# Optimization experiments

Hardware: AMD Instinct MI355X
Metric: run time of the kernel (lower is better)

Reference implementation:

```python
import jax, jax.numpy as jnp
import numpy as np

NUM_ROUTING = 3


def squash(v, axis=-1):
    s2 = jnp.sum(jnp.square(v), axis=axis, keepdims=True)
    scale = s2 / (1.0 + s2) / jnp.sqrt(s2 + 1e-7)
    return scale * v


def setup_inputs() -> dict:
    key = jax.random.key(0)
    k1, k2 = jax.random.split(key)
    B, I, D_in, J, D_out = 64, 2304, 8, 32, 16
    inputs = jax.random.normal(k1, (B, I, D_in), dtype=jnp.float32)
    # keras random_uniform(-1, 1)
    W = jax.random.uniform(k2, (I, J, D_in, D_out), dtype=jnp.float32, minval=-1.0, maxval=1.0)
    b0 = jnp.zeros((I, J), dtype=jnp.float32)
    return {"inputs": inputs, "W": W, "b0": b0}


def reference(inputs, W, b0):
    B = inputs.shape[0]
    I, J = b0.shape
    # u_hat[b,i,j,e] = inputs[b,i,:] @ W[i,j,:,e]  -> [B, I, J, E]
    u_hat = jnp.einsum('bid,ijde->bije', inputs, W)
    b = jnp.broadcast_to(b0[None], (B, I, J))
    V = None
    for it in range(NUM_ROUTING):
        c = jax.nn.softmax(b, axis=-1)                      # [B, I, J]
        S = jnp.einsum('bij,bije->bje', c, u_hat)           # [B, J, E]
        V = squash(S)
        if it != NUM_ROUTING - 1:
            b = b + jnp.einsum('bje,bije->bij', V, u_hat)   # agreement update
    return V
```

## Files before the change

### kernel.cpp

```cpp
#include <hip/hip_runtime.h>
#include <hip/hip_fp16.h>

#define I_DIM 2304
#define J_DIM 32
#define D_IN  8
#define E_DIM 16
#define B_DIM 64
#define BJE   (B_DIM * J_DIM * E_DIM)
#define HBJE  (BJE / 2)
#define NC7   256
#define CH7   (I_DIM / NC7)
#define TILEW 4096

typedef const __attribute__((address_space(1))) char* gcp_t;
typedef __attribute__((address_space(3)))       char* lcp_t;

#define DPP_ADD(s, ctrl) ((s) + __int_as_float(__builtin_amdgcn_update_dpp( \
    0, __float_as_int(s), (ctrl), 0xF, 0xF, true)))

template <bool FIRST>
__global__ __launch_bounds__(256, 2) void caps_pass_v22(
    const float* __restrict__ x,
    const float* __restrict__ W,
    const float* __restrict__ b0,
    const float* __restrict__ Vacc,
    __half2* __restrict__ partial)
{
    const int tid   = threadIdx.x;
    const int wv    = __builtin_amdgcn_readfirstlane(tid >> 6);
    const int wvx   = tid >> 6;
    const int lane  = tid & 63;
    const int jj    = lane & 31;
    const int eh    = lane >> 5;
    const int km    = jj & 15;
    const int chunk = blockIdx.x & (NC7 - 1);
    const int qb    = blockIdx.x >> 8;
    const int i0    = chunk * CH7;
    const int bloc0 = wv * 4;
    const int bbase = qb * 16 + bloc0;
    const int bxb   = qb * 16 + wvx * 4;

    __shared__ float Ws[2][TILEW];

    auto stage = [&](int buf, int itile) {
        const char* wt = (const char*)(W + (size_t)itile * TILEW);
#pragma unroll
        for (int r = 0; r < 4; ++r) {
            const int g    = (wv * 4 + r) * 64 + lane;
            const int srcu = (g & ~31) | ((g & 31) ^ ((g >> 5) & 15));
            __builtin_amdgcn_global_load_lds(
                (gcp_t)(wt + (size_t)srcu * 16),
                (lcp_t)((char*)&Ws[buf][(wv * 4 + r) * 256]),
                16, 0, 0);
        }
    };

    stage(0, i0);

    float vacc[4][8];
    if constexpr (!FIRST) {
#pragma unroll
        for (int bb = 0; bb < 4; ++bb) {
            const float* vp = Vacc + ((size_t)((bbase + bb) * J_DIM + jj)) * E_DIM + eh * 8;
            const float4 v0 = *(const float4*)vp;
            const float4 v1 = *(const float4*)(vp + 4);
            vacc[bb][0]=v0.x; vacc[bb][1]=v0.y; vacc[bb][2]=v0.z; vacc[bb][3]=v0.w;
            vacc[bb][4]=v1.x; vacc[bb][5]=v1.y; vacc[bb][6]=v1.z; vacc[bb][7]=v1.w;
        }
    }

    float Sacc[4][8];
#pragma unroll
    for (int bb = 0; bb < 4; ++bb)
#pragma unroll
        for (int e = 0; e < 8; ++e) Sacc[bb][e] = 0.f;

    __syncthreads();

    int cur = 0;
    for (int ii = 0; ii < CH7; ++ii) {
        const int i = i0 + ii;
        if (ii + 1 < CH7) stage(cur ^ 1, i + 1);

        const float b0v = b0[i * J_DIM + jj];

        const float* wb = &Ws[cur][0];

        float uh[4][8];
#pragma unroll
        for (int bb = 0; bb < 4; ++bb)
#pragma unroll
            for (int e = 0; e < 8; ++e) uh[bb][e] = 0.f;

        {
            float xq[4][4];
#pragma unroll
            for (int bb = 0; bb < 4; ++bb) {
                const float4 t = *(const float4*)(x + ((size_t)(bxb + bb) * I_DIM + i) * D_IN);
                xq[bb][0]=t.x; xq[bb][1]=t.y; xq[bb][2]=t.z; xq[bb][3]=t.w;
            }
            float4 w[8];
#pragma unroll
            for (int d = 0; d < 4; ++d) {
                const int u0 = (d << 2) | (eh << 1);
                w[2*d]   = *(const float4*)&wb[jj * 128 + (((u0    ) ^ km) << 2)];
                w[2*d+1] = *(const float4*)&wb[jj * 128 + (((u0 | 1) ^ km) << 2)];
            }
#pragma unroll
            for (int d = 0; d < 4; ++d) {
                const float4 wlo = w[2*d], whi = w[2*d+1];
#pragma unroll
                for (int bb = 0; bb < 4; ++bb) {
                    const float xv = xq[bb][d];
                    uh[bb][0] = fmaf(xv, wlo.x, uh[bb][0]);
                    uh[bb][1] = fmaf(xv, wlo.y, uh[bb][1]);
                    uh[bb][2] = fmaf(xv, wlo.z, uh[bb][2]);
                    uh[bb][3] = fmaf(xv, wlo.w, uh[bb][3]);
                    uh[bb][4] = fmaf(xv, whi.x, uh[bb][4]);
                    uh[bb][5] = fmaf(xv, whi.y, uh[bb][5]);
                    uh[bb][6] = fmaf(xv, whi.z, uh[bb][6]);
                    uh[bb][7] = fmaf(xv, whi.w, uh[bb][7]);
                }
            }
        }
        {
            float xq[4][4];
#pragma unroll
            for (int bb = 0; bb < 4; ++bb) {
                const float4 t = *(const float4*)(x + ((size_t)(bxb + bb) * I_DIM + i) * D_IN + 4);
                xq[bb][0]=t.x; xq[bb][1]=t.y; xq[bb][2]=t.z; xq[bb][3]=t.w;
            }
            float4 w[8];
#pragma unroll
            for (int d = 4; d < 8; ++d) {
                const int u0 = (d << 2) | (eh << 1);
                w[2*(d-4)]   = *(const float4*)&wb[jj * 128 + (((u0    ) ^ km) << 2)];
                w[2*(d-4)+1] = *(const float4*)&wb[jj * 128 + (((u0 | 1) ^ km) << 2)];
            }
#pragma unroll
            for (int d = 0; d < 4; ++d) {
                const float4 wlo = w[2*d], whi = w[2*d+1];
#pragma unroll
                for (int bb = 0; bb < 4; ++bb) {
                    const float xv = xq[bb][d];
                    uh[bb][0] = fmaf(xv, wlo.x, uh[bb][0]);
                    uh[bb][1] = fmaf(xv, wlo.y, uh[bb][1]);
                    uh[bb][2] = fmaf(xv, wlo.z, uh[bb][2]);
                    uh[bb][3] = fmaf(xv, wlo.w, uh[bb][3]);
                    uh[bb][4] = fmaf(xv, whi.x, uh[bb][4]);
                    uh[bb][5] = fmaf(xv, whi.y, uh[bb][5]);
                    uh[bb][6] = fmaf(xv, whi.z, uh[bb][6]);
                    uh[bb][7] = fmaf(xv, whi.w, uh[bb][7]);
                }
            }
        }

#pragma unroll
        for (int bb = 0; bb < 4; ++bb) {
            float l;
            if constexpr (FIRST) {
                l = b0v;
            } else {
                float l0 = 0.f, l1 = 0.f;
#pragma unroll
                for (int e = 0; e < 8; e += 2) {
                    l0 = fmaf(vacc[bb][e],     uh[bb][e],     l0);
                    l1 = fmaf(vacc[bb][e + 1], uh[bb][e + 1], l1);
                }
                float lg = l0 + l1;
                lg += __shfl_xor(lg, 32);
                l = b0v + lg;
            }

            const float p = __expf(l);
            float s = p;
            s = DPP_ADD(s, 0xB1);
            s = DPP_ADD(s, 0x4E);
            s = DPP_ADD(s, 0x124);
            s = DPP_ADD(s, 0x128);
            s += __shfl_xor(s, 16);
            const float c = p * __builtin_amdgcn_rcpf(s);

#pragma unroll
            for (int e = 0; e < 8; ++e) Sacc[bb][e] = fmaf(c, uh[bb][e], Sacc[bb][e]);
        }

        __syncthreads();
        cur ^= 1;
    }

#pragma unroll
    for (int bb = 0; bb < 4; ++bb) {
        __half2 h0 = __floats2half2_rn(Sacc[bb][0], Sacc[bb][1]);
        __half2 h1 = __floats2half2_rn(Sacc[bb][2], Sacc[bb][3]);
        __half2 h2 = __floats2half2_rn(Sacc[bb][4], Sacc[bb][5]);
        __half2 h3 = __floats2half2_rn(Sacc[bb][6], Sacc[bb][7]);
        __half2* pp = partial + (size_t)chunk * HBJE
                    + ((size_t)((bbase + bb) * J_DIM + jj)) * (E_DIM / 2) + eh * 4;
        int4 pk = make_int4(*(int*)&h0, *(int*)&h1, *(int*)&h2, *(int*)&h3);
        *(int4*)pp = pk;
    }
}

__global__ __launch_bounds__(256) void reduce_squash(
    const __half2* __restrict__ partial, float* __restrict__ Vacc,
    float* __restrict__ out, const int nc, const int first_it, const int final_it)
{
    const int t = blockIdx.x * blockDim.x + threadIdx.x;
    float ax0=0.f,ay0=0.f,ax1=0.f,ay1=0.f,ax2=0.f,ay2=0.f,ax3=0.f,ay3=0.f;
    for (int c = 0; c < nc; c += 4) {
        const float2 f0 = __half22float2(partial[(size_t)(c+0) * HBJE + t]);
        const float2 f1 = __half22float2(partial[(size_t)(c+1) * HBJE + t]);
        const float2 f2 = __half22float2(partial[(size_t)(c+2) * HBJE + t]);
        const float2 f3 = __half22float2(partial[(size_t)(c+3) * HBJE + t]);
        ax0 += f0.x; ay0 += f0.y;
        ax1 += f1.x; ay1 += f1.y;
        ax2 += f2.x; ay2 += f2.y;
        ax3 += f3.x; ay3 += f3.y;
    }
    const float sx = (ax0 + ax1) + (ax2 + ax3);
    const float sy = (ay0 + ay1) + (ay2 + ay3);

    float s2 = sx * sx + sy * sy;
#pragma unroll
    for (int k = 4; k >= 1; k >>= 1) s2 += __shfl_xor(s2, k);
    const float scale = s2 / (1.f + s2) * rsqrtf(s2 + 1e-7f);
    const float2 v = make_float2(scale * sx, scale * sy);
    if (final_it)      *(float2*)(out  + 2 * (size_t)t) = v;
    else if (first_it) *(float2*)(Vacc + 2 * (size_t)t) = v;
    else {
        float2 old = *(const float2*)(Vacc + 2 * (size_t)t);
        *(float2*)(Vacc + 2 * (size_t)t) = make_float2(old.x + v.x, old.y + v.y);
    }
}

extern "C" void kernel_launch(void* const* d_in, const int* in_sizes, int n_in,
                              void* d_out, int out_size, void* d_ws, size_t ws_size,
                              hipStream_t stream) {
    const float* x  = (const float*)d_in[0];
    const float* W  = (const float*)d_in[1];
    const float* b0 = (const float*)d_in[2];
    float* out = (float*)d_out;

    __half2* partial = (__half2*)d_ws;
    float*   Vacc    = (float*)(partial + (size_t)NC7 * HBJE);

    caps_pass_v22<true><<<NC7 * 4, 256, 0, stream>>>(x, W, b0, Vacc, partial);
    reduce_squash<<<HBJE / 256, 256, 0, stream>>>(partial, Vacc, out, NC7, 1, 0);

    caps_pass_v22<false><<<NC7 * 4, 256, 0, stream>>>(x, W, b0, Vacc, partial);
    reduce_squash<<<HBJE / 256, 256, 0, stream>>>(partial, Vacc, out, NC7, 0, 0);

    caps_pass_v22<false><<<NC7 * 4, 256, 0, stream>>>(x, W, b0, Vacc, partial);
    reduce_squash<<<HBJE / 256, 256, 0, stream>>>(partial, Vacc, out, NC7, 0, 1);
}
```

Measured before the change: 162.5 us.

## Cache u_hat in fp16 workspace and reuse it in later routing passes

The first routing pass now writes the predicted vectors u_hat to a global fp16 buffer. A new kernel for the remaining two passes reads them back instead of recomputing u_hat from W and x. This removes the per-pass matmul recompute and the W tile staging. In exchange, about 150 MB of writes and two full reads hit HBM, fp16 rounding of u_hat enters the agreement logits, and the workspace must be large enough.

```diff
diff --git a/kernel.cpp b/kernel.cpp
--- a/kernel.cpp
+++ b/kernel.cpp
@@ -18,13 +18,13 @@
 #define DPP_ADD(s, ctrl) ((s) + __int_as_float(__builtin_amdgcn_update_dpp( \
     0, __float_as_int(s), (ctrl), 0xF, 0xF, true)))
 
-template <bool FIRST>
-__global__ __launch_bounds__(256, 2) void caps_pass_v22(
+
+__global__ __launch_bounds__(256, 2) void caps_pass0(
     const float* __restrict__ x,
     const float* __restrict__ W,
     const float* __restrict__ b0,
-    const float* __restrict__ Vacc,
-    __half2* __restrict__ partial)
+    __half2* __restrict__ partial,
+    int4* __restrict__ uh_buf)
 {
     const int tid   = threadIdx.x;
     const int wv    = __builtin_amdgcn_readfirstlane(tid >> 6);
@@ -57,18 +57,6 @@
 
     stage(0, i0);
 
-    float vacc[4][8];
-    if constexpr (!FIRST) {
-#pragma unroll
-        for (int bb = 0; bb < 4; ++bb) {
-            const float* vp = Vacc + ((size_t)((bbase + bb) * J_DIM + jj)) * E_DIM + eh * 8;
-            const float4 v0 = *(const float4*)vp;
-            const float4 v1 = *(const float4*)(vp + 4);
-            vacc[bb][0]=v0.x; vacc[bb][1]=v0.y; vacc[bb][2]=v0.z; vacc[bb][3]=v0.w;
-            vacc[bb][4]=v1.x; vacc[bb][5]=v1.y; vacc[bb][6]=v1.z; vacc[bb][7]=v1.w;
-        }
-    }
-
     float Sacc[4][8];
 #pragma unroll
     for (int bb = 0; bb < 4; ++bb)
@@ -83,7 +71,6 @@
         if (ii + 1 < CH7) stage(cur ^ 1, i + 1);
 
         const float b0v = b0[i * J_DIM + jj];
-
         const float* wb = &Ws[cur][0];
 
         float uh[4][8];
@@ -155,22 +142,108 @@
             }
         }
 
+        {
+            int4* ub = uh_buf + (size_t)i * 4096 + qb * 1024 + wv * 256 + lane;
+#pragma unroll
+            for (int bb = 0; bb < 4; ++bb) {
+                __half2 h0 = __floats2half2_rn(uh[bb][0], uh[bb][1]);
+                __half2 h1 = __floats2half2_rn(uh[bb][2], uh[bb][3]);
+                __half2 h2 = __floats2half2_rn(uh[bb][4], uh[bb][5]);
+                __half2 h3 = __floats2half2_rn(uh[bb][6], uh[bb][7]);
+                ub[bb * 64] = make_int4(*(int*)&h0, *(int*)&h1, *(int*)&h2, *(int*)&h3);
+            }
+        }
+
+        {
+            const float p = __expf(b0v);
+            float s = p;
+            s = DPP_ADD(s, 0xB1);
+            s = DPP_ADD(s, 0x4E);
+            s = DPP_ADD(s, 0x124);
+            s = DPP_ADD(s, 0x128);
+            s += __shfl_xor(s, 16);
+            const float c = p * __builtin_amdgcn_rcpf(s);
+#pragma unroll
+            for (int bb = 0; bb < 4; ++bb)
+#pragma unroll
+                for (int e = 0; e < 8; ++e) Sacc[bb][e] = fmaf(c, uh[bb][e], Sacc[bb][e]);
+        }
+
+        __syncthreads();
+        cur ^= 1;
+    }
+
+#pragma unroll
+    for (int bb = 0; bb < 4; ++bb) {
+        __half2 h0 = __floats2half2_rn(Sacc[bb][0], Sacc[bb][1]);
+        __half2 h1 = __floats2half2_rn(Sacc[bb][2], Sacc[bb][3]);
+        __half2 h2 = __floats2half2_rn(Sacc[bb][4], Sacc[bb][5]);
+        __half2 h3 = __floats2half2_rn(Sacc[bb][6], Sacc[bb][7]);
+        __half2* pp = partial + (size_t)chunk * HBJE
+                    + ((size_t)((bbase + bb) * J_DIM + jj)) * (E_DIM / 2) + eh * 4;
+        *(int4*)pp = make_int4(*(int*)&h0, *(int*)&h1, *(int*)&h2, *(int*)&h3);
+    }
+}
+
+__global__ __launch_bounds__(256, 2) void caps_pass_uh(
+    const int4* __restrict__ uh_buf,
+    const float* __restrict__ b0,
+    const float* __restrict__ Vacc,
+    __half2* __restrict__ partial)
+{
+    const int tid   = threadIdx.x;
+    const int wvx   = tid >> 6;
+    const int lane  = tid & 63;
+    const int jj    = lane & 31;
+    const int eh    = lane >> 5;
+    const int chunk = blockIdx.x & (NC7 - 1);
+    const int qb    = blockIdx.x >> 8;
+    const int i0    = chunk * CH7;
+    const int bbase = qb * 16 + wvx * 4;
+
+    float vacc[4][8];
+#pragma unroll
+    for (int bb = 0; bb < 4; ++bb) {
+        const float* vp = Vacc + ((size_t)((bbase + bb) * J_DIM + jj)) * E_DIM + eh * 8;
+        const float4 v0 = *(const float4*)vp;
+        const float4 v1 = *(const float4*)(vp + 4);
+        vacc[bb][0]=v0.x; vacc[bb][1]=v0.y; vacc[bb][2]=v0.z; vacc[bb][3]=v0.w;
+        vacc[bb][4]=v1.x; vacc[bb][5]=v1.y; vacc[bb][6]=v1.z; vacc[bb][7]=v1.w;
+    }
+
+    float Sacc[4][8];
+#pragma unroll
+    for (int bb = 0; bb < 4; ++bb)
+#pragma unroll
+        for (int e = 0; e < 8; ++e) Sacc[bb][e] = 0.f;
+
+#pragma unroll
+    for (int ii = 0; ii < CH7; ++ii) {
+        const int i = i0 + ii;
+        const float b0v = b0[i * J_DIM + jj];
+
+        const int4* ub = uh_buf + (size_t)i * 4096 + qb * 1024 + wvx * 256 + lane;
+        int4 u[4];
+#pragma unroll
+        for (int bb = 0; bb < 4; ++bb) u[bb] = ub[bb * 64];
+
 #pragma unroll
         for (int bb = 0; bb < 4; ++bb) {
-            float l;
-            if constexpr (FIRST) {
-                l = b0v;
-            } else {
-                float l0 = 0.f, l1 = 0.f;
-#pragma unroll
-                for (int e = 0; e < 8; e += 2) {
-                    l0 = fmaf(vacc[bb][e],     uh[bb][e],     l0);
-                    l1 = fmaf(vacc[bb][e + 1], uh[bb][e + 1], l1);
-                }
-                float lg = l0 + l1;
-                lg += __shfl_xor(lg, 32);
-                l = b0v + lg;
-            }
+            const float2 f0 = __half22float2(*(const __half2*)&u[bb].x);
+            const float2 f1 = __half22float2(*(const __half2*)&u[bb].y);
+            const float2 f2 = __half22float2(*(const __half2*)&u[bb].z);
+            const float2 f3 = __half22float2(*(const __half2*)&u[bb].w);
+            const float uhf[8] = {f0.x, f0.y, f1.x, f1.y, f2.x, f2.y, f3.x, f3.y};
+
+            float l0 = 0.f, l1 = 0.f;
+#pragma unroll
+            for (int e = 0; e < 8; e += 2) {
+                l0 = fmaf(vacc[bb][e],     uhf[e],     l0);
+                l1 = fmaf(vacc[bb][e + 1], uhf[e + 1], l1);
+            }
+            float lg = l0 + l1;
+            lg += __shfl_xor(lg, 32);
+            const float l = b0v + lg;
 
             const float p = __expf(l);
             float s = p;
@@ -182,11 +255,8 @@
             const float c = p * __builtin_amdgcn_rcpf(s);
 
 #pragma unroll
-            for (int e = 0; e < 8; ++e) Sacc[bb][e] = fmaf(c, uh[bb][e], Sacc[bb][e]);
-        }
-
-        __syncthreads();
-        cur ^= 1;
+            for (int e = 0; e < 8; ++e) Sacc[bb][e] = fmaf(c, uhf[e], Sacc[bb][e]);
+        }
     }
 
 #pragma unroll
@@ -197,8 +267,7 @@
         __half2 h3 = __floats2half2_rn(Sacc[bb][6], Sacc[bb][7]);
         __half2* pp = partial + (size_t)chunk * HBJE
                     + ((size_t)((bbase + bb) * J_DIM + jj)) * (E_DIM / 2) + eh * 4;
-        int4 pk = make_int4(*(int*)&h0, *(int*)&h1, *(int*)&h2, *(int*)&h3);
-        *(int4*)pp = pk;
+        *(int4*)pp = make_int4(*(int*)&h0, *(int*)&h1, *(int*)&h2, *(int*)&h3);
     }
 }
 
@@ -244,13 +313,14 @@
 
     __half2* partial = (__half2*)d_ws;
     float*   Vacc    = (float*)(partial + (size_t)NC7 * HBJE);
-
-    caps_pass_v22<true><<<NC7 * 4, 256, 0, stream>>>(x, W, b0, Vacc, partial);
+    int4*    uh_buf  = (int4*)(Vacc + BJE);
+
+    caps_pass0<<<NC7 * 4, 256, 0, stream>>>(x, W, b0, partial, uh_buf);
     reduce_squash<<<HBJE / 256, 256, 0, stream>>>(partial, Vacc, out, NC7, 1, 0);
 
-    caps_pass_v22<false><<<NC7 * 4, 256, 0, stream>>>(x, W, b0, Vacc, partial);
+    caps_pass_uh<<<NC7 * 4, 256, 0, stream>>>(uh_buf, b0, Vacc, partial);
     reduce_squash<<<HBJE / 256, 256, 0, stream>>>(partial, Vacc, out, NC7, 0, 0);
 
-    caps_pass_v22<false><<<NC7 * 4, 256, 0, stream>>>(x, W, b0, Vacc, partial);
+    caps_pass_uh<<<NC7 * 4, 256, 0, stream>>>(uh_buf, b0, Vacc, partial);
     reduce_squash<<<HBJE / 256, 256, 0, stream>>>(partial, Vacc, out, NC7, 0, 1);
 }
```

Result: slower. 169.2 us (+4.1%).
